# Optimization experiments

Measured on AMD Instinct MI355X. Metric: run time of the kernel, lower is better.

The kernel has to match this reference:

```python
import jax, jax.numpy as jnp
import numpy as np

T, B, H, L = 64, 128, 256, 2  # steps/stack_size, batch, hidden, layers


def setup_inputs() -> dict:
    key = jax.random.key(0)
    ks = jax.random.split(key, 6)
    s = 1.0 / np.sqrt(H)
    x = jax.random.normal(ks[0], (T, B, H), dtype=jnp.float32)
    ops = jax.random.randint(ks[1], (T, B), 0, 2, dtype=jnp.int32)  # push=1, hold=0
    W_ih = jax.random.uniform(ks[2], (L, 4 * H, H), jnp.float32, -s, s)
    W_hh = jax.random.uniform(ks[3], (L, 4 * H, H), jnp.float32, -s, s)
    b_ih = jax.random.uniform(ks[4], (L, 4 * H), jnp.float32, -s, s)
    b_hh = jax.random.uniform(ks[5], (L, 4 * H), jnp.float32, -s, s)
    return {"x": x, "ops": ops, "W_ih": W_ih, "W_hh": W_hh, "b_ih": b_ih, "b_hh": b_hh}


def reference(x, ops, W_ih, W_hh, b_ih, b_hh):
    T_, B_, H_ = x.shape
    L_ = W_ih.shape[0]
    bidx = jnp.arange(B_)

    def cell(xt, h_prev, c_prev):
        # multi-layer LSTM cell; layer l>0 takes layer l-1 hidden as input (dropout=0)
        inp = xt
        hs, cs = [], []
        for l in range(L_):
            gates = inp @ W_ih[l].T + b_ih[l] + h_prev[..., l] @ W_hh[l].T + b_hh[l]
            i, f, g, o = jnp.split(gates, 4, axis=-1)
            c = jax.nn.sigmoid(f) * c_prev[..., l] + jax.nn.sigmoid(i) * jnp.tanh(g)
            h = jax.nn.sigmoid(o) * jnp.tanh(c)
            hs.append(h)
            cs.append(c)
            inp = h
        return jnp.stack(hs, axis=-1), jnp.stack(cs, axis=-1)  # (B, H, L)

    def step(carry, xt_op):
        hstack, cstack, pos = carry  # stacks: (T+1, B, H, L), pos: (B,)
        xt, opt = xt_op
        h_prev = hstack[pos, bidx]  # gather top-of-stack, (B, H, L)
        c_prev = cstack[pos, bidx]
        nh, nc = cell(xt, h_prev, c_prev)
        # hold_or_push writes at pos+1 for every batch element, then pos += op
        hstack = hstack.at[pos + 1, bidx].set(nh)
        cstack = cstack.at[pos + 1, bidx].set(nc)
        pos = pos + opt
        return (hstack, cstack, pos), nh[..., -1]  # last-layer hidden output

    hs0 = jnp.zeros((T_ + 1, B_, H_, L_), dtype=x.dtype)
    cs0 = jnp.zeros((T_ + 1, B_, H_, L_), dtype=x.dtype)
    pos0 = jnp.zeros((B_,), dtype=jnp.int32)
    _, outs = jax.lax.scan(step, (hs0, cs0, pos0), (x, ops))
    return outs  # (T, B, H)
```

## Files before the change

kernel.cpp:

```cpp
#include <hip/hip_runtime.h>
#include <hip/hip_fp16.h>
#include <cstddef>

#define TT 64
#define BB 128
#define HH 256
#define G4 1024
#define BLK 256
#define NBG 32
#define NHG 16

#define OFF_XG     0u
#define OFF_WTIH0  8388608u
#define OFF_HX0    8650752u
#define OFF_HX1    8716288u

__device__ __forceinline__ float sigf(float x) { return 1.0f / (1.0f + expf(-x)); }

typedef _Float16 h2v __attribute__((ext_vector_type(2)));

__device__ __forceinline__ float dot2acc(unsigned w, unsigned h, float acc) {
#if __has_builtin(__builtin_amdgcn_fdot2)
  return __builtin_amdgcn_fdot2(__builtin_bit_cast(h2v, w),
                                __builtin_bit_cast(h2v, h), acc, false);
#else
  __half2 wv = *(__half2*)&w, hv = *(__half2*)&h;
  float2 wf = __half22float2(wv), hf = __half22float2(hv);
  return fmaf(wf.x, hf.x, fmaf(wf.y, hf.y, acc));
#endif
}

__device__ __forceinline__ unsigned packh2(float e, float o) {
  return (unsigned)__half_as_ushort(__float2half(e)) |
         ((unsigned)__half_as_ushort(__float2half(o)) << 16);
}

__global__ void transpose1(const float* __restrict__ W_ih, float* __restrict__ ws) {
  __shared__ float tile[32][33];
  float* dst = ws + OFF_WTIH0;
  const int g0 = blockIdx.x * 32, k0 = blockIdx.y * 32;
  const int tx = threadIdx.x, ty = threadIdx.y;
#pragma unroll
  for (int i = 0; i < 32; i += 8)
    tile[ty + i][tx] = W_ih[(size_t)(g0 + ty + i) * HH + k0 + tx];
  __syncthreads();
#pragma unroll
  for (int i = 0; i < 32; i += 8)
    dst[(size_t)(k0 + ty + i) * G4 + g0 + tx] = tile[tx][ty + i];
}

__global__ void xg_kernel(const float* __restrict__ x,
                          const float* __restrict__ b_ih,
                          float* __restrict__ ws) {
  const float* __restrict__ WTih0 = ws + OFF_WTIH0;
  float* __restrict__ Xg = ws + OFF_XG;
  const int r0 = blockIdx.x * 16;
  const int g = blockIdx.y * 256 + threadIdx.x;
  __shared__ float xs[16][HH];
  for (int i = threadIdx.x; i < 16 * HH; i += 256)
    xs[i >> 8][i & 255] = x[(size_t)(r0 + (i >> 8)) * HH + (i & 255)];
  __syncthreads();
  float acc[16];
  const float bias = b_ih[g];
#pragma unroll
  for (int r = 0; r < 16; ++r) acc[r] = bias;
  for (int k = 0; k < HH; ++k) {
    const float w = WTih0[(size_t)k * G4 + g];
#pragma unroll
    for (int r = 0; r < 16; ++r) acc[r] = fmaf(xs[r][k], w, acc[r]);
  }
  const int hg = (g >> 4) & 15;
  const int lc = ((g >> 8) << 4) | (g & 15);
#pragma unroll
  for (int r = 0; r < 16; ++r) {
    const int rr = r0 + r;
    const int t = rr >> 7, b = rr & 127;
    Xg[(((size_t)t * NHG + hg) * 128 + b) * 64 + lc] = acc[r];
  }
}

__global__ void __launch_bounds__(BLK, 2)
seq7(const float* __restrict__ W_ih,
     const float* __restrict__ W_hh,
     const float* __restrict__ b_ih,
     const float* __restrict__ b_hh,
     const int* __restrict__ ops,
     float* __restrict__ ws,
     float* __restrict__ out) {
  const int bg = blockIdx.x & 31;
  const int hg = blockIdx.x >> 5;
  const int tid = threadIdx.x;
  const int kq = tid & 7;
  const int c2 = tid >> 3;

  __shared__ float XgL[TT * 256];
  __shared__ unsigned hp0[512];
  __shared__ unsigned hp1[512];
  __shared__ unsigned h0c[512];
  __shared__ float gat[256];
  __shared__ int opsA[TT * 4];

  unsigned wr0[32], wr1[32], wr2[32];
  {
    const float* s0 = W_hh;
    const float* s1 = W_ih + (size_t)G4 * HH;
    const float* s2 = W_hh + (size_t)G4 * HH;
#pragma unroll
    for (int j = 0; j < 2; ++j) {
      const int lc = c2 * 2 + j;
      const int g = ((lc >> 4) << 8) + hg * 16 + (lc & 15);
      const float* p0 = s0 + (size_t)g * HH + kq * 32;
      const float* p1 = s1 + (size_t)g * HH + kq * 32;
      const float* p2 = s2 + (size_t)g * HH + kq * 32;
#pragma unroll
      for (int i = 0; i < 16; ++i) {
        wr0[j * 16 + i] = packh2(p0[2 * i], p0[2 * i + 1]);
        wr1[j * 16 + i] = packh2(p1[2 * i], p1[2 * i + 1]);
        wr2[j * 16 + i] = packh2(p2[2 * i], p2[2 * i + 1]);
      }
    }
  }
  float bias0r[2], bias1r[2];
#pragma unroll
  for (int j = 0; j < 2; ++j) {
    const int lc = c2 * 2 + j;
    const int g = ((lc >> 4) << 8) + hg * 16 + (lc & 15);
    bias0r[j] = b_hh[g];
    bias1r[j] = b_ih[G4 + g] + b_hh[G4 + g];
  }
  for (int i = tid; i < TT * 64; i += BLK) {
    const int t = i >> 6, r = i & 63;
    ((float4*)XgL)[i] = *(const float4*)(
        ws + OFF_XG + (((size_t)t * NHG + hg) * 128 + bg * 4) * 64 + r * 4);
  }
  for (int i = tid; i < TT * 4; i += BLK)
    opsA[i] = ops[(i >> 2) * BB + bg * 4 + (i & 3)];
  for (int i = tid; i < 512; i += BLK) { hp0[i] = 0u; hp1[i] = 0u; }

  unsigned long long* __restrict__ Hx0 = (unsigned long long*)(ws + OFF_HX0);
  unsigned long long* __restrict__ Hx1 = (unsigned long long*)(ws + OFF_HX1);
  float cp0 = 0.f, cp1 = 0.f;
  __syncthreads();

  for (int t = 0; t < TT; ++t) {
    const int par = t & 1;

    float a0[4][2];
#pragma unroll
    for (int b = 0; b < 4; ++b) {
      const uint4 x0 = *(const uint4*)&hp0[b * 128 + kq * 16];
      const uint4 x1 = *(const uint4*)&hp0[b * 128 + kq * 16 + 4];
      const uint4 x2 = *(const uint4*)&hp0[b * 128 + kq * 16 + 8];
      const uint4 x3 = *(const uint4*)&hp0[b * 128 + kq * 16 + 12];
      const unsigned hh[16] = {x0.x, x0.y, x0.z, x0.w, x1.x, x1.y, x1.z, x1.w,
                               x2.x, x2.y, x2.z, x2.w, x3.x, x3.y, x3.z, x3.w};
#pragma unroll
      for (int j = 0; j < 2; ++j) {
        float a = 0.f;
#pragma unroll
        for (int i = 0; i < 16; ++i) a = dot2acc(wr0[j * 16 + i], hh[i], a);
        a0[b][j] = a;
      }
    }
#pragma unroll
    for (int m = 1; m <= 4; m <<= 1)
#pragma unroll
      for (int b = 0; b < 4; ++b) {
        a0[b][0] += __shfl_xor(a0[b][0], m, 64);
        a0[b][1] += __shfl_xor(a0[b][1], m, 64);
      }
    if (kq == 0) {
#pragma unroll
      for (int b = 0; b < 4; ++b)
        *(float2*)&gat[b * 64 + c2 * 2] =
            make_float2(a0[b][0] + bias0r[0], a0[b][1] + bias0r[1]);
    }
    __syncthreads();

    if (tid < 64) {
      const int b = tid >> 4, r = tid & 15;
      const float* xg = &XgL[t * 256 + b * 64];
      const float* gt = &gat[b * 64];
      const float ig = gt[r] + xg[r],           fg = gt[16 + r] + xg[16 + r];
      const float gg = gt[32 + r] + xg[32 + r], og = gt[48 + r] + xg[48 + r];
      const float c = sigf(fg) * cp0 + sigf(ig) * tanhf(gg);
      const float h = sigf(og) * tanhf(c);
      if (opsA[t * 4 + b]) cp0 = c;
      const float ho = __shfl_xor(h, 1, 64);
      if (!(r & 1)) {
        const unsigned long long v =
            (unsigned long long)(unsigned)(t + 1) |
            ((unsigned long long)packh2(h, ho) << 32);
        __hip_atomic_store(
            Hx0 + ((size_t)par * NBG + bg) * 512 + b * 128 + hg * 8 + (r >> 1),
            v, __ATOMIC_RELAXED, __HIP_MEMORY_SCOPE_AGENT);
      }
    }

    {
      const unsigned long long* s0 = Hx0 + ((size_t)par * NBG + bg) * 512;
      const unsigned tagA = (unsigned)(t + 1);
#pragma unroll
      for (int i = 0; i < 2; ++i) {
        const int idx = tid + i * 256;
        const int b = idx >> 7, k2 = idx & 127;
        unsigned long long v;
        int spins = 0;
        for (;;) {
          v = __hip_atomic_load(s0 + idx, __ATOMIC_RELAXED,
                                __HIP_MEMORY_SCOPE_AGENT);
          if ((unsigned)v == tagA) break;
          if (++spins > (1 << 18)) break;
          __builtin_amdgcn_s_sleep(1);
        }
        const unsigned pay = (unsigned)(v >> 32);
        h0c[b * 128 + k2] = pay;
        if (opsA[t * 4 + b]) hp0[b * 128 + k2] = pay;
      }
      if (t > 0) {
        const unsigned long long* s1 = Hx1 + ((size_t)(par ^ 1) * NBG + bg) * 512;
        const unsigned tagB = (unsigned)t;
#pragma unroll
        for (int i = 0; i < 2; ++i) {
          const int idx = tid + i * 256;
          const int b = idx >> 7, k2 = idx & 127;
          unsigned long long v;
          int spins = 0;
          for (;;) {
            v = __hip_atomic_load(s1 + idx, __ATOMIC_RELAXED,
                                  __HIP_MEMORY_SCOPE_AGENT);
            if ((unsigned)v == tagB) break;
            if (++spins > (1 << 18)) break;
            __builtin_amdgcn_s_sleep(1);
          }
          if (opsA[(t - 1) * 4 + b]) hp1[b * 128 + k2] = (unsigned)(v >> 32);
        }
      }
    }
    __syncthreads();

    float a1[4][2];
#pragma unroll
    for (int b = 0; b < 4; ++b) {
      const uint4 c0 = *(const uint4*)&h0c[b * 128 + kq * 16];
      const uint4 c1 = *(const uint4*)&h0c[b * 128 + kq * 16 + 4];
      const uint4 c2v = *(const uint4*)&h0c[b * 128 + kq * 16 + 8];
      const uint4 c3 = *(const uint4*)&h0c[b * 128 + kq * 16 + 12];
      const uint4 q0 = *(const uint4*)&hp1[b * 128 + kq * 16];
      const uint4 q1 = *(const uint4*)&hp1[b * 128 + kq * 16 + 4];
      const uint4 q2 = *(const uint4*)&hp1[b * 128 + kq * 16 + 8];
      const uint4 q3 = *(const uint4*)&hp1[b * 128 + kq * 16 + 12];
      const unsigned hc[16] = {c0.x, c0.y, c0.z, c0.w, c1.x, c1.y, c1.z, c1.w,
                               c2v.x, c2v.y, c2v.z, c2v.w, c3.x, c3.y, c3.z, c3.w};
      const unsigned hq[16] = {q0.x, q0.y, q0.z, q0.w, q1.x, q1.y, q1.z, q1.w,
                               q2.x, q2.y, q2.z, q2.w, q3.x, q3.y, q3.z, q3.w};
#pragma unroll
      for (int j = 0; j < 2; ++j) {
        float a = 0.f;
#pragma unroll
        for (int i = 0; i < 16; ++i) {
          a = dot2acc(wr1[j * 16 + i], hc[i], a);
          a = dot2acc(wr2[j * 16 + i], hq[i], a);
        }
        a1[b][j] = a;
      }
    }
#pragma unroll
    for (int m = 1; m <= 4; m <<= 1)
#pragma unroll
      for (int b = 0; b < 4; ++b) {
        a1[b][0] += __shfl_xor(a1[b][0], m, 64);
        a1[b][1] += __shfl_xor(a1[b][1], m, 64);
      }
    if (kq == 0) {
#pragma unroll
      for (int b = 0; b < 4; ++b)
        *(float2*)&gat[b * 64 + c2 * 2] =
            make_float2(a1[b][0] + bias1r[0], a1[b][1] + bias1r[1]);
    }
    __syncthreads();

    if (tid < 64) {
      const int b = tid >> 4, r = tid & 15;
      const float* gt = &gat[b * 64];
      const float ig = gt[r],      fg = gt[16 + r];
      const float gg = gt[32 + r], og = gt[48 + r];
      const float c = sigf(fg) * cp1 + sigf(ig) * tanhf(gg);
      const float h = sigf(og) * tanhf(c);
      if (opsA[t * 4 + b]) cp1 = c;
      out[((size_t)t * BB + bg * 4 + b) * HH + hg * 16 + r] = h;
      const float ho = __shfl_xor(h, 1, 64);
      if (!(r & 1)) {
        const unsigned long long v =
            (unsigned long long)(unsigned)(t + 1) |
            ((unsigned long long)packh2(h, ho) << 32);
        __hip_atomic_store(
            Hx1 + ((size_t)par * NBG + bg) * 512 + b * 128 + hg * 8 + (r >> 1),
            v, __ATOMIC_RELAXED, __HIP_MEMORY_SCOPE_AGENT);
      }
    }
    __syncthreads();
  }
}

extern "C" void kernel_launch(void* const* d_in, const int* in_sizes, int n_in,
                              void* d_out, int out_size, void* d_ws, size_t ws_size,
                              hipStream_t stream) {
  const float* x    = (const float*)d_in[0];
  const int*   ops  = (const int*)d_in[1];
  const float* W_ih = (const float*)d_in[2];
  const float* W_hh = (const float*)d_in[3];
  const float* b_ih = (const float*)d_in[4];
  const float* b_hh = (const float*)d_in[5];
  float* out = (float*)d_out;
  float* ws  = (float*)d_ws;

  transpose1<<<dim3(32, 8), dim3(32, 8), 0, stream>>>(W_ih, ws);
  xg_kernel<<<dim3(512, 4), 256, 0, stream>>>(x, b_ih, ws);
  seq7<<<512, BLK, 0, stream>>>(W_ih, W_hh, b_ih, b_hh, ops, ws, out);
}
```

Measured before the change: 561.2 us.

## Split batch across twice as many persistent blocks with interleaved K layout

Halves the batch slice per block (4 to 2 rows), doubling the grid to 1024 blocks and raising launch bounds to 4 blocks per CU, so per-step matvec and LDS work per block shrinks. The K-slice assignment per lane is changed to an interleaved pattern so the uint4 LDS reads of adjacent lanes are contiguous, reducing bank conflicts. The spin-wait now polls the layer-1 exchange before the layer-0 exchange with one element per thread. The cost is twice as many blocks holding the same weights in registers (weights loaded twice), more cross-block flag traffic, and reliance on all 1024 blocks being co-resident for the spin-based synchronization not to deadlock.

Measured after the change: 893.6 us. 1.59x slower.

```diff
diff --git a/kernel.cpp b/kernel.cpp
--- a/kernel.cpp
+++ b/kernel.cpp
@@ -7,7 +7,7 @@
 #define HH 256
 #define G4 1024
 #define BLK 256
-#define NBG 32
+#define NBG 64
 #define NHG 16
 
 #define OFF_XG     0u
@@ -79,26 +79,26 @@
   }
 }
 
-__global__ void __launch_bounds__(BLK, 2)
-seq7(const float* __restrict__ W_ih,
+__global__ void __launch_bounds__(BLK, 4)
+seq8(const float* __restrict__ W_ih,
      const float* __restrict__ W_hh,
      const float* __restrict__ b_ih,
      const float* __restrict__ b_hh,
      const int* __restrict__ ops,
      float* __restrict__ ws,
      float* __restrict__ out) {
-  const int bg = blockIdx.x & 31;
-  const int hg = blockIdx.x >> 5;
+  const int bg = blockIdx.x & 63;
+  const int hg = blockIdx.x >> 6;
   const int tid = threadIdx.x;
   const int kq = tid & 7;
   const int c2 = tid >> 3;
 
-  __shared__ float XgL[TT * 256];
-  __shared__ unsigned hp0[512];
-  __shared__ unsigned hp1[512];
-  __shared__ unsigned h0c[512];
-  __shared__ float gat[256];
-  __shared__ int opsA[TT * 4];
+  __shared__ float XgL[TT * 128];
+  __shared__ unsigned hp0[256];
+  __shared__ unsigned hp1[256];
+  __shared__ unsigned h0c[256];
+  __shared__ float gat[128];
+  __shared__ int opsA[TT * 2];
 
   unsigned wr0[32], wr1[32], wr2[32];
   {
@@ -109,15 +109,18 @@
     for (int j = 0; j < 2; ++j) {
       const int lc = c2 * 2 + j;
       const int g = ((lc >> 4) << 8) + hg * 16 + (lc & 15);
-      const float* p0 = s0 + (size_t)g * HH + kq * 32;
-      const float* p1 = s1 + (size_t)g * HH + kq * 32;
-      const float* p2 = s2 + (size_t)g * HH + kq * 32;
-#pragma unroll
-      for (int i = 0; i < 16; ++i) {
-        wr0[j * 16 + i] = packh2(p0[2 * i], p0[2 * i + 1]);
-        wr1[j * 16 + i] = packh2(p1[2 * i], p1[2 * i + 1]);
-        wr2[j * 16 + i] = packh2(p2[2 * i], p2[2 * i + 1]);
-      }
+#pragma unroll
+      for (int s = 0; s < 4; ++s)
+#pragma unroll
+        for (int i = 0; i < 4; ++i) {
+          const int k2 = s * 32 + kq * 4 + i;
+          const float* p0 = s0 + (size_t)g * HH + 2 * k2;
+          const float* p1 = s1 + (size_t)g * HH + 2 * k2;
+          const float* p2 = s2 + (size_t)g * HH + 2 * k2;
+          wr0[j * 16 + s * 4 + i] = packh2(p0[0], p0[1]);
+          wr1[j * 16 + s * 4 + i] = packh2(p1[0], p1[1]);
+          wr2[j * 16 + s * 4 + i] = packh2(p2[0], p2[1]);
+        }
     }
   }
   float bias0r[2], bias1r[2];
@@ -128,14 +131,14 @@
     bias0r[j] = b_hh[g];
     bias1r[j] = b_ih[G4 + g] + b_hh[G4 + g];
   }
-  for (int i = tid; i < TT * 64; i += BLK) {
-    const int t = i >> 6, r = i & 63;
+  for (int i = tid; i < TT * 32; i += BLK) {
+    const int t = i >> 5, r = i & 31;
     ((float4*)XgL)[i] = *(const float4*)(
-        ws + OFF_XG + (((size_t)t * NHG + hg) * 128 + bg * 4) * 64 + r * 4);
-  }
-  for (int i = tid; i < TT * 4; i += BLK)
-    opsA[i] = ops[(i >> 2) * BB + bg * 4 + (i & 3)];
-  for (int i = tid; i < 512; i += BLK) { hp0[i] = 0u; hp1[i] = 0u; }
+        ws + OFF_XG + (((size_t)t * NHG + hg) * 128 + bg * 2) * 64 + r * 4);
+  }
+  for (int i = tid; i < TT * 2; i += BLK)
+    opsA[i] = ops[(i >> 1) * BB + bg * 2 + (i & 1)];
+  for (int i = tid; i < 256; i += BLK) { hp0[i] = 0u; hp1[i] = 0u; }
 
   unsigned long long* __restrict__ Hx0 = (unsigned long long*)(ws + OFF_HX0);
   unsigned long long* __restrict__ Hx1 = (unsigned long long*)(ws + OFF_HX1);
@@ -145,13 +148,13 @@
   for (int t = 0; t < TT; ++t) {
     const int par = t & 1;
 
-    float a0[4][2];
-#pragma unroll
-    for (int b = 0; b < 4; ++b) {
-      const uint4 x0 = *(const uint4*)&hp0[b * 128 + kq * 16];
-      const uint4 x1 = *(const uint4*)&hp0[b * 128 + kq * 16 + 4];
-      const uint4 x2 = *(const uint4*)&hp0[b * 128 + kq * 16 + 8];
-      const uint4 x3 = *(const uint4*)&hp0[b * 128 + kq * 16 + 12];
+    float a0[2][2];
+#pragma unroll
+    for (int b = 0; b < 2; ++b) {
+      const uint4 x0 = *(const uint4*)&hp0[b * 128 + 0 * 32 + kq * 4];
+      const uint4 x1 = *(const uint4*)&hp0[b * 128 + 1 * 32 + kq * 4];
+      const uint4 x2 = *(const uint4*)&hp0[b * 128 + 2 * 32 + kq * 4];
+      const uint4 x3 = *(const uint4*)&hp0[b * 128 + 3 * 32 + kq * 4];
       const unsigned hh[16] = {x0.x, x0.y, x0.z, x0.w, x1.x, x1.y, x1.z, x1.w,
                                x2.x, x2.y, x2.z, x2.w, x3.x, x3.y, x3.z, x3.w};
 #pragma unroll
@@ -165,49 +168,61 @@
 #pragma unroll
     for (int m = 1; m <= 4; m <<= 1)
 #pragma unroll
-      for (int b = 0; b < 4; ++b) {
+      for (int b = 0; b < 2; ++b) {
         a0[b][0] += __shfl_xor(a0[b][0], m, 64);
         a0[b][1] += __shfl_xor(a0[b][1], m, 64);
       }
     if (kq == 0) {
 #pragma unroll
-      for (int b = 0; b < 4; ++b)
+      for (int b = 0; b < 2; ++b)
         *(float2*)&gat[b * 64 + c2 * 2] =
             make_float2(a0[b][0] + bias0r[0], a0[b][1] + bias0r[1]);
     }
     __syncthreads();
 
-    if (tid < 64) {
+    if (tid < 32) {
       const int b = tid >> 4, r = tid & 15;
-      const float* xg = &XgL[t * 256 + b * 64];
+      const float* xg = &XgL[t * 128 + b * 64];
       const float* gt = &gat[b * 64];
       const float ig = gt[r] + xg[r],           fg = gt[16 + r] + xg[16 + r];
       const float gg = gt[32 + r] + xg[32 + r], og = gt[48 + r] + xg[48 + r];
       const float c = sigf(fg) * cp0 + sigf(ig) * tanhf(gg);
       const float h = sigf(og) * tanhf(c);
-      if (opsA[t * 4 + b]) cp0 = c;
+      if (opsA[t * 2 + b]) cp0 = c;
       const float ho = __shfl_xor(h, 1, 64);
       if (!(r & 1)) {
         const unsigned long long v =
             (unsigned long long)(unsigned)(t + 1) |
             ((unsigned long long)packh2(h, ho) << 32);
         __hip_atomic_store(
-            Hx0 + ((size_t)par * NBG + bg) * 512 + b * 128 + hg * 8 + (r >> 1),
+            Hx0 + ((size_t)par * NBG + bg) * 256 + b * 128 + hg * 8 + (r >> 1),
             v, __ATOMIC_RELAXED, __HIP_MEMORY_SCOPE_AGENT);
       }
     }
 
     {
-      const unsigned long long* s0 = Hx0 + ((size_t)par * NBG + bg) * 512;
-      const unsigned tagA = (unsigned)(t + 1);
-#pragma unroll
-      for (int i = 0; i < 2; ++i) {
-        const int idx = tid + i * 256;
-        const int b = idx >> 7, k2 = idx & 127;
+      const int b = tid >> 7, k2 = tid & 127;
+      if (t > 0) {
+        const unsigned long long* s1 = Hx1 + ((size_t)(par ^ 1) * NBG + bg) * 256;
+        const unsigned tagB = (unsigned)t;
         unsigned long long v;
         int spins = 0;
         for (;;) {
-          v = __hip_atomic_load(s0 + idx, __ATOMIC_RELAXED,
+          v = __hip_atomic_load(s1 + tid, __ATOMIC_RELAXED,
+                                __HIP_MEMORY_SCOPE_AGENT);
+          if ((unsigned)v == tagB) break;
+          if (++spins > (1 << 18)) break;
+          __builtin_amdgcn_s_sleep(1);
+        }
+        if (opsA[(t - 1) * 2 + b]) hp1[b * 128 + k2] = (unsigned)(v >> 32);
+      }
+      {
+        const unsigned long long* s0 = Hx0 + ((size_t)par * NBG + bg) * 256;
+        const unsigned tagA = (unsigned)(t + 1);
+        unsigned long long v;
+        int spins = 0;
+        for (;;) {
+          v = __hip_atomic_load(s0 + tid, __ATOMIC_RELAXED,
                                 __HIP_MEMORY_SCOPE_AGENT);
           if ((unsigned)v == tagA) break;
           if (++spins > (1 << 18)) break;
@@ -215,41 +230,22 @@
         }
         const unsigned pay = (unsigned)(v >> 32);
         h0c[b * 128 + k2] = pay;
-        if (opsA[t * 4 + b]) hp0[b * 128 + k2] = pay;
-      }
-      if (t > 0) {
-        const unsigned long long* s1 = Hx1 + ((size_t)(par ^ 1) * NBG + bg) * 512;
-        const unsigned tagB = (unsigned)t;
-#pragma unroll
-        for (int i = 0; i < 2; ++i) {
-          const int idx = tid + i * 256;
-          const int b = idx >> 7, k2 = idx & 127;
-          unsigned long long v;
-          int spins = 0;
-          for (;;) {
-            v = __hip_atomic_load(s1 + idx, __ATOMIC_RELAXED,
-                                  __HIP_MEMORY_SCOPE_AGENT);
-            if ((unsigned)v == tagB) break;
-            if (++spins > (1 << 18)) break;
-            __builtin_amdgcn_s_sleep(1);
-          }
-          if (opsA[(t - 1) * 4 + b]) hp1[b * 128 + k2] = (unsigned)(v >> 32);
-        }
+        if (opsA[t * 2 + b]) hp0[b * 128 + k2] = pay;
       }
     }
     __syncthreads();
 
-    float a1[4][2];
-#pragma unroll
-    for (int b = 0; b < 4; ++b) {
-      const uint4 c0 = *(const uint4*)&h0c[b * 128 + kq * 16];
-      const uint4 c1 = *(const uint4*)&h0c[b * 128 + kq * 16 + 4];
-      const uint4 c2v = *(const uint4*)&h0c[b * 128 + kq * 16 + 8];
-      const uint4 c3 = *(const uint4*)&h0c[b * 128 + kq * 16 + 12];
-      const uint4 q0 = *(const uint4*)&hp1[b * 128 + kq * 16];
-      const uint4 q1 = *(const uint4*)&hp1[b * 128 + kq * 16 + 4];
-      const uint4 q2 = *(const uint4*)&hp1[b * 128 + kq * 16 + 8];
-      const uint4 q3 = *(const uint4*)&hp1[b * 128 + kq * 16 + 12];
+    float a1[2][2];
+#pragma unroll
+    for (int b = 0; b < 2; ++b) {
+      const uint4 c0 = *(const uint4*)&h0c[b * 128 + 0 * 32 + kq * 4];
+      const uint4 c1 = *(const uint4*)&h0c[b * 128 + 1 * 32 + kq * 4];
+      const uint4 c2v = *(const uint4*)&h0c[b * 128 + 2 * 32 + kq * 4];
+      const uint4 c3 = *(const uint4*)&h0c[b * 128 + 3 * 32 + kq * 4];
+      const uint4 q0 = *(const uint4*)&hp1[b * 128 + 0 * 32 + kq * 4];
+      const uint4 q1 = *(const uint4*)&hp1[b * 128 + 1 * 32 + kq * 4];
+      const uint4 q2 = *(const uint4*)&hp1[b * 128 + 2 * 32 + kq * 4];
+      const uint4 q3 = *(const uint4*)&hp1[b * 128 + 3 * 32 + kq * 4];
       const unsigned hc[16] = {c0.x, c0.y, c0.z, c0.w, c1.x, c1.y, c1.z, c1.w,
                                c2v.x, c2v.y, c2v.z, c2v.w, c3.x, c3.y, c3.z, c3.w};
       const unsigned hq[16] = {q0.x, q0.y, q0.z, q0.w, q1.x, q1.y, q1.z, q1.w,
@@ -268,34 +264,34 @@
 #pragma unroll
     for (int m = 1; m <= 4; m <<= 1)
 #pragma unroll
-      for (int b = 0; b < 4; ++b) {
+      for (int b = 0; b < 2; ++b) {
         a1[b][0] += __shfl_xor(a1[b][0], m, 64);
         a1[b][1] += __shfl_xor(a1[b][1], m, 64);
       }
     if (kq == 0) {
 #pragma unroll
-      for (int b = 0; b < 4; ++b)
+      for (int b = 0; b < 2; ++b)
         *(float2*)&gat[b * 64 + c2 * 2] =
             make_float2(a1[b][0] + bias1r[0], a1[b][1] + bias1r[1]);
     }
     __syncthreads();
 
-    if (tid < 64) {
+    if (tid < 32) {
       const int b = tid >> 4, r = tid & 15;
       const float* gt = &gat[b * 64];
       const float ig = gt[r],      fg = gt[16 + r];
       const float gg = gt[32 + r], og = gt[48 + r];
       const float c = sigf(fg) * cp1 + sigf(ig) * tanhf(gg);
       const float h = sigf(og) * tanhf(c);
-      if (opsA[t * 4 + b]) cp1 = c;
-      out[((size_t)t * BB + bg * 4 + b) * HH + hg * 16 + r] = h;
+      if (opsA[t * 2 + b]) cp1 = c;
+      out[((size_t)t * BB + bg * 2 + b) * HH + hg * 16 + r] = h;
       const float ho = __shfl_xor(h, 1, 64);
       if (!(r & 1)) {
         const unsigned long long v =
             (unsigned long long)(unsigned)(t + 1) |
             ((unsigned long long)packh2(h, ho) << 32);
         __hip_atomic_store(
-            Hx1 + ((size_t)par * NBG + bg) * 512 + b * 128 + hg * 8 + (r >> 1),
+            Hx1 + ((size_t)par * NBG + bg) * 256 + b * 128 + hg * 8 + (r >> 1),
             v, __ATOMIC_RELAXED, __HIP_MEMORY_SCOPE_AGENT);
       }
     }
@@ -317,5 +313,5 @@
 
   transpose1<<<dim3(32, 8), dim3(32, 8), 0, stream>>>(W_ih, ws);
   xg_kernel<<<dim3(512, 4), 256, 0, stream>>>(x, b_ih, ws);
-  seq7<<<512, BLK, 0, stream>>>(W_ih, W_hh, b_ih, b_hh, ops, ws, out);
-}
+  seq8<<<1024, BLK, 0, stream>>>(W_ih, W_hh, b_ih, b_hh, ops, ws, out);
+}
```

## Split hidden dimension across twice as many persistent blocks with fewer weights each

Applied to the files above, without the earlier changes.

The persistent sequential kernel now launches 1024 blocks instead of 512, each owning 8 hidden units instead of 16. Each thread keeps half as many packed fp16 weights in registers, and the launch bound is raised to 4 blocks per SIMD so all blocks can be co-resident. The per-block shared-memory copy of the input projection is replaced by a per-step global load, and the layer-1 flag wait is reordered ahead of the layer-0 wait. The aim is to shorten the per-step dot-product critical path. In exchange, twice as many blocks must poll the flag exchange buffers each step, and every block must stay resident or the spin waits will stall.

New measurement: 589.7 us. 5.1% more time.

```diff
diff --git a/kernel.cpp b/kernel.cpp
--- a/kernel.cpp
+++ b/kernel.cpp
@@ -8,7 +8,7 @@
 #define G4 1024
 #define BLK 256
 #define NBG 32
-#define NHG 16
+#define NHG 32
 
 #define OFF_XG     0u
 #define OFF_WTIH0  8388608u
@@ -69,18 +69,18 @@
 #pragma unroll
     for (int r = 0; r < 16; ++r) acc[r] = fmaf(xs[r][k], w, acc[r]);
   }
-  const int hg = (g >> 4) & 15;
-  const int lc = ((g >> 8) << 4) | (g & 15);
+  const int hg = (g >> 3) & 31;
+  const int lc = ((g >> 8) << 3) | (g & 7);
 #pragma unroll
   for (int r = 0; r < 16; ++r) {
     const int rr = r0 + r;
     const int t = rr >> 7, b = rr & 127;
-    Xg[(((size_t)t * NHG + hg) * 128 + b) * 64 + lc] = acc[r];
-  }
-}
-
-__global__ void __launch_bounds__(BLK, 2)
-seq7(const float* __restrict__ W_ih,
+    Xg[(((size_t)t * NHG + hg) * 128 + b) * 32 + lc] = acc[r];
+  }
+}
+
+__global__ void __launch_bounds__(BLK, 4)
+seq9(const float* __restrict__ W_ih,
      const float* __restrict__ W_hh,
      const float* __restrict__ b_ih,
      const float* __restrict__ b_hh,
@@ -91,48 +91,36 @@
   const int hg = blockIdx.x >> 5;
   const int tid = threadIdx.x;
   const int kq = tid & 7;
-  const int c2 = tid >> 3;
-
-  __shared__ float XgL[TT * 256];
+  const int cc = tid >> 3;
+
   __shared__ unsigned hp0[512];
   __shared__ unsigned hp1[512];
   __shared__ unsigned h0c[512];
-  __shared__ float gat[256];
+  __shared__ float gat[128];
+  __shared__ float xgb[128];
   __shared__ int opsA[TT * 4];
 
-  unsigned wr0[32], wr1[32], wr2[32];
+  unsigned wr0[16], wr1[16], wr2[16];
+  const int g = ((cc >> 3) << 8) + hg * 8 + (cc & 7);
   {
     const float* s0 = W_hh;
     const float* s1 = W_ih + (size_t)G4 * HH;
     const float* s2 = W_hh + (size_t)G4 * HH;
 #pragma unroll
-    for (int j = 0; j < 2; ++j) {
-      const int lc = c2 * 2 + j;
-      const int g = ((lc >> 4) << 8) + hg * 16 + (lc & 15);
-      const float* p0 = s0 + (size_t)g * HH + kq * 32;
-      const float* p1 = s1 + (size_t)g * HH + kq * 32;
-      const float* p2 = s2 + (size_t)g * HH + kq * 32;
-#pragma unroll
-      for (int i = 0; i < 16; ++i) {
-        wr0[j * 16 + i] = packh2(p0[2 * i], p0[2 * i + 1]);
-        wr1[j * 16 + i] = packh2(p1[2 * i], p1[2 * i + 1]);
-        wr2[j * 16 + i] = packh2(p2[2 * i], p2[2 * i + 1]);
-      }
-    }
-  }
-  float bias0r[2], bias1r[2];
-#pragma unroll
-  for (int j = 0; j < 2; ++j) {
-    const int lc = c2 * 2 + j;
-    const int g = ((lc >> 4) << 8) + hg * 16 + (lc & 15);
-    bias0r[j] = b_hh[g];
-    bias1r[j] = b_ih[G4 + g] + b_hh[G4 + g];
-  }
-  for (int i = tid; i < TT * 64; i += BLK) {
-    const int t = i >> 6, r = i & 63;
-    ((float4*)XgL)[i] = *(const float4*)(
-        ws + OFF_XG + (((size_t)t * NHG + hg) * 128 + bg * 4) * 64 + r * 4);
-  }
+    for (int s = 0; s < 4; ++s)
+#pragma unroll
+      for (int i = 0; i < 4; ++i) {
+        const int k2 = s * 32 + kq * 4 + i;
+        const float* p0 = s0 + (size_t)g * HH + 2 * k2;
+        const float* p1 = s1 + (size_t)g * HH + 2 * k2;
+        const float* p2 = s2 + (size_t)g * HH + 2 * k2;
+        wr0[s * 4 + i] = packh2(p0[0], p0[1]);
+        wr1[s * 4 + i] = packh2(p1[0], p1[1]);
+        wr2[s * 4 + i] = packh2(p2[0], p2[1]);
+      }
+  }
+  const float bias0 = b_hh[g];
+  const float bias1 = b_ih[G4 + g] + b_hh[G4 + g];
   for (int i = tid; i < TT * 4; i += BLK)
     opsA[i] = ops[(i >> 2) * BB + bg * 4 + (i & 3)];
   for (int i = tid; i < 512; i += BLK) { hp0[i] = 0u; hp1[i] = 0u; }
@@ -145,44 +133,42 @@
   for (int t = 0; t < TT; ++t) {
     const int par = t & 1;
 
-    float a0[4][2];
+    float xgv = 0.f;
+    if (tid < 128)
+      xgv = ws[OFF_XG + (((size_t)t * NHG + hg) * 128 + bg * 4 + (tid >> 5)) * 32 +
+               (tid & 31)];
+
+    float a0[4];
 #pragma unroll
     for (int b = 0; b < 4; ++b) {
-      const uint4 x0 = *(const uint4*)&hp0[b * 128 + kq * 16];
-      const uint4 x1 = *(const uint4*)&hp0[b * 128 + kq * 16 + 4];
-      const uint4 x2 = *(const uint4*)&hp0[b * 128 + kq * 16 + 8];
-      const uint4 x3 = *(const uint4*)&hp0[b * 128 + kq * 16 + 12];
-      const unsigned hh[16] = {x0.x, x0.y, x0.z, x0.w, x1.x, x1.y, x1.z, x1.w,
-                               x2.x, x2.y, x2.z, x2.w, x3.x, x3.y, x3.z, x3.w};
-#pragma unroll
-      for (int j = 0; j < 2; ++j) {
-        float a = 0.f;
-#pragma unroll
-        for (int i = 0; i < 16; ++i) a = dot2acc(wr0[j * 16 + i], hh[i], a);
-        a0[b][j] = a;
-      }
+      float a = 0.f;
+#pragma unroll
+      for (int s = 0; s < 4; ++s) {
+        const uint4 hx = *(const uint4*)&hp0[b * 128 + s * 32 + kq * 4];
+        a = dot2acc(wr0[s * 4 + 0], hx.x, a);
+        a = dot2acc(wr0[s * 4 + 1], hx.y, a);
+        a = dot2acc(wr0[s * 4 + 2], hx.z, a);
+        a = dot2acc(wr0[s * 4 + 3], hx.w, a);
+      }
+      a0[b] = a;
     }
 #pragma unroll
     for (int m = 1; m <= 4; m <<= 1)
 #pragma unroll
-      for (int b = 0; b < 4; ++b) {
-        a0[b][0] += __shfl_xor(a0[b][0], m, 64);
-        a0[b][1] += __shfl_xor(a0[b][1], m, 64);
-      }
+      for (int b = 0; b < 4; ++b) a0[b] += __shfl_xor(a0[b], m, 64);
     if (kq == 0) {
 #pragma unroll
-      for (int b = 0; b < 4; ++b)
-        *(float2*)&gat[b * 64 + c2 * 2] =
-            make_float2(a0[b][0] + bias0r[0], a0[b][1] + bias0r[1]);
-    }
-    __syncthreads();
-
-    if (tid < 64) {
-      const int b = tid >> 4, r = tid & 15;
-      const float* xg = &XgL[t * 256 + b * 64];
-      const float* gt = &gat[b * 64];
-      const float ig = gt[r] + xg[r],           fg = gt[16 + r] + xg[16 + r];
-      const float gg = gt[32 + r] + xg[32 + r], og = gt[48 + r] + xg[48 + r];
+      for (int b = 0; b < 4; ++b) gat[b * 32 + cc] = a0[b] + bias0;
+    }
+    if (tid < 128) xgb[tid] = xgv;
+    __syncthreads();
+
+    if (tid < 32) {
+      const int b = tid >> 3, r = tid & 7;
+      const float* gt = &gat[b * 32];
+      const float* xg = &xgb[b * 32];
+      const float ig = gt[r] + xg[r],           fg = gt[8 + r] + xg[8 + r];
+      const float gg = gt[16 + r] + xg[16 + r], og = gt[24 + r] + xg[24 + r];
       const float c = sigf(fg) * cp0 + sigf(ig) * tanhf(gg);
       const float h = sigf(og) * tanhf(c);
       if (opsA[t * 4 + b]) cp0 = c;
@@ -192,18 +178,32 @@
             (unsigned long long)(unsigned)(t + 1) |
             ((unsigned long long)packh2(h, ho) << 32);
         __hip_atomic_store(
-            Hx0 + ((size_t)par * NBG + bg) * 512 + b * 128 + hg * 8 + (r >> 1),
+            Hx0 + ((size_t)par * NBG + bg) * 512 + b * 128 + hg * 4 + (r >> 1),
             v, __ATOMIC_RELAXED, __HIP_MEMORY_SCOPE_AGENT);
       }
     }
 
-    {
-      const unsigned long long* s0 = Hx0 + ((size_t)par * NBG + bg) * 512;
-      const unsigned tagA = (unsigned)(t + 1);
-#pragma unroll
-      for (int i = 0; i < 2; ++i) {
-        const int idx = tid + i * 256;
-        const int b = idx >> 7, k2 = idx & 127;
+#pragma unroll
+    for (int i = 0; i < 2; ++i) {
+      const int idx = tid + i * 256;
+      const int b = idx >> 7, k2 = idx & 127;
+      if (t > 0) {
+        const unsigned long long* s1 = Hx1 + ((size_t)(par ^ 1) * NBG + bg) * 512;
+        const unsigned tagB = (unsigned)t;
+        unsigned long long v;
+        int spins = 0;
+        for (;;) {
+          v = __hip_atomic_load(s1 + idx, __ATOMIC_RELAXED,
+                                __HIP_MEMORY_SCOPE_AGENT);
+          if ((unsigned)v == tagB) break;
+          if (++spins > (1 << 18)) break;
+          __builtin_amdgcn_s_sleep(1);
+        }
+        if (opsA[(t - 1) * 4 + b]) hp1[b * 128 + k2] = (unsigned)(v >> 32);
+      }
+      {
+        const unsigned long long* s0 = Hx0 + ((size_t)par * NBG + bg) * 512;
+        const unsigned tagA = (unsigned)(t + 1);
         unsigned long long v;
         int spins = 0;
         for (;;) {
@@ -217,85 +217,54 @@
         h0c[b * 128 + k2] = pay;
         if (opsA[t * 4 + b]) hp0[b * 128 + k2] = pay;
       }
-      if (t > 0) {
-        const unsigned long long* s1 = Hx1 + ((size_t)(par ^ 1) * NBG + bg) * 512;
-        const unsigned tagB = (unsigned)t;
-#pragma unroll
-        for (int i = 0; i < 2; ++i) {
-          const int idx = tid + i * 256;
-          const int b = idx >> 7, k2 = idx & 127;
-          unsigned long long v;
-          int spins = 0;
-          for (;;) {
-            v = __hip_atomic_load(s1 + idx, __ATOMIC_RELAXED,
-                                  __HIP_MEMORY_SCOPE_AGENT);
-            if ((unsigned)v == tagB) break;
-            if (++spins > (1 << 18)) break;
-            __builtin_amdgcn_s_sleep(1);
-          }
-          if (opsA[(t - 1) * 4 + b]) hp1[b * 128 + k2] = (unsigned)(v >> 32);
-        }
-      }
-    }
-    __syncthreads();
-
-    float a1[4][2];
+    }
+    __syncthreads();
+
+    float a1[4];
 #pragma unroll
     for (int b = 0; b < 4; ++b) {
-      const uint4 c0 = *(const uint4*)&h0c[b * 128 + kq * 16];
-      const uint4 c1 = *(const uint4*)&h0c[b * 128 + kq * 16 + 4];
-      const uint4 c2v = *(const uint4*)&h0c[b * 128 + kq * 16 + 8];
-      const uint4 c3 = *(const uint4*)&h0c[b * 128 + kq * 16 + 12];
-      const uint4 q0 = *(const uint4*)&hp1[b * 128 + kq * 16];
-      const uint4 q1 = *(const uint4*)&hp1[b * 128 + kq * 16 + 4];
-      const uint4 q2 = *(const uint4*)&hp1[b * 128 + kq * 16 + 8];
-      const uint4 q3 = *(const uint4*)&hp1[b * 128 + kq * 16 + 12];
-      const unsigned hc[16] = {c0.x, c0.y, c0.z, c0.w, c1.x, c1.y, c1.z, c1.w,
-                               c2v.x, c2v.y, c2v.z, c2v.w, c3.x, c3.y, c3.z, c3.w};
-      const unsigned hq[16] = {q0.x, q0.y, q0.z, q0.w, q1.x, q1.y, q1.z, q1.w,
-                               q2.x, q2.y, q2.z, q2.w, q3.x, q3.y, q3.z, q3.w};
-#pragma unroll
-      for (int j = 0; j < 2; ++j) {
-        float a = 0.f;
-#pragma unroll
-        for (int i = 0; i < 16; ++i) {
-          a = dot2acc(wr1[j * 16 + i], hc[i], a);
-          a = dot2acc(wr2[j * 16 + i], hq[i], a);
-        }
-        a1[b][j] = a;
-      }
+      float a = 0.f;
+#pragma unroll
+      for (int s = 0; s < 4; ++s) {
+        const uint4 hc = *(const uint4*)&h0c[b * 128 + s * 32 + kq * 4];
+        const uint4 hq = *(const uint4*)&hp1[b * 128 + s * 32 + kq * 4];
+        a = dot2acc(wr1[s * 4 + 0], hc.x, a);
+        a = dot2acc(wr1[s * 4 + 1], hc.y, a);
+        a = dot2acc(wr1[s * 4 + 2], hc.z, a);
+        a = dot2acc(wr1[s * 4 + 3], hc.w, a);
+        a = dot2acc(wr2[s * 4 + 0], hq.x, a);
+        a = dot2acc(wr2[s * 4 + 1], hq.y, a);
+        a = dot2acc(wr2[s * 4 + 2], hq.z, a);
+        a = dot2acc(wr2[s * 4 + 3], hq.w, a);
+      }
+      a1[b] = a;
     }
 #pragma unroll
     for (int m = 1; m <= 4; m <<= 1)
 #pragma unroll
-      for (int b = 0; b < 4; ++b) {
-        a1[b][0] += __shfl_xor(a1[b][0], m, 64);
-        a1[b][1] += __shfl_xor(a1[b][1], m, 64);
-      }
+      for (int b = 0; b < 4; ++b) a1[b] += __shfl_xor(a1[b], m, 64);
     if (kq == 0) {
 #pragma unroll
-      for (int b = 0; b < 4; ++b)
-        *(float2*)&gat[b * 64 + c2 * 2] =
-            make_float2(a1[b][0] + bias1r[0], a1[b][1] + bias1r[1]);
-    }
-    __syncthreads();
-
-    if (tid < 64) {
-      const int b = tid >> 4, r = tid & 15;
-      const float* gt = &gat[b * 64];
-      const float ig = gt[r],      fg = gt[16 + r];
-      const float gg = gt[32 + r], og = gt[48 + r];
+      for (int b = 0; b < 4; ++b) gat[b * 32 + cc] = a1[b] + bias1;
+    }
+    __syncthreads();
+
+    if (tid < 32) {
+      const int b = tid >> 3, r = tid & 7;
+      const float* gt = &gat[b * 32];
+      const float ig = gt[r],      fg = gt[8 + r];
+      const float gg = gt[16 + r], og = gt[24 + r];
       const float c = sigf(fg) * cp1 + sigf(ig) * tanhf(gg);
       const float h = sigf(og) * tanhf(c);
       if (opsA[t * 4 + b]) cp1 = c;
-      out[((size_t)t * BB + bg * 4 + b) * HH + hg * 16 + r] = h;
+      out[((size_t)t * BB + bg * 4 + b) * HH + hg * 8 + r] = h;
       const float ho = __shfl_xor(h, 1, 64);
       if (!(r & 1)) {
         const unsigned long long v =
             (unsigned long long)(unsigned)(t + 1) |
             ((unsigned long long)packh2(h, ho) << 32);
         __hip_atomic_store(
-            Hx1 + ((size_t)par * NBG + bg) * 512 + b * 128 + hg * 8 + (r >> 1),
+            Hx1 + ((size_t)par * NBG + bg) * 512 + b * 128 + hg * 4 + (r >> 1),
             v, __ATOMIC_RELAXED, __HIP_MEMORY_SCOPE_AGENT);
       }
     }
@@ -317,5 +286,5 @@
 
   transpose1<<<dim3(32, 8), dim3(32, 8), 0, stream>>>(W_ih, ws);
   xg_kernel<<<dim3(512, 4), 256, 0, stream>>>(x, b_ih, ws);
-  seq7<<<512, BLK, 0, stream>>>(W_ih, W_hh, b_ih, b_hh, ops, ws, out);
-}
+  seq9<<<1024, BLK, 0, stream>>>(W_ih, W_hh, b_ih, b_hh, ops, ws, out);
+}
```
